# Optimization experiments

Hardware: AMD Instinct MI355X
Metric: run time of the kernel (lower is better)

Reference implementation:

```python
import jax, jax.numpy as jnp
import numpy as np

B, C, T, O = 64, 256, 4096, 256
LEVELS = 5


def setup_inputs() -> dict:
    key = jax.random.key(0)
    ks = jax.random.split(key, 10)
    s = 0.05  # weight scale, avoids tanh/sigmoid saturation
    inputs = jax.random.normal(ks[0], (B, C, T), dtype=jnp.float32)
    # original-resolution lengths; k = lens // 2**(levels-1) in [1, T]
    lens = jax.random.randint(ks[1], (B,), 16, T * 2 ** (LEVELS - 1) + 1, dtype=jnp.int32)
    return {
        "inputs": inputs,
        "lens": lens,
        "levels": LEVELS,
        "W_tanh": jax.random.normal(ks[2], (C, C), dtype=jnp.float32) * s,
        "b_tanh": jax.random.normal(ks[3], (C,), dtype=jnp.float32) * s,
        "W_sigm": jax.random.normal(ks[4], (C, C), dtype=jnp.float32) * s,
        "b_sigm": jax.random.normal(ks[5], (C,), dtype=jnp.float32) * s,
        "W_w": jax.random.normal(ks[6], (O, C), dtype=jnp.float32) * s,
        "b_w": jax.random.normal(ks[7], (O,), dtype=jnp.float32) * s,
        "W_final": jax.random.normal(ks[8], (O, C), dtype=jnp.float32) * s,
        "b_final": jax.random.normal(ks[9], (O,), dtype=jnp.float32) * s,
    }


def _conv1x1(x, W, b):
    # Conv1d with kernel_size=1: [B,C,T] x [O,C] -> [B,O,T]
    return jnp.einsum('oc,bct->bot', W, x) + b[None, :, None]


def reference(inputs, lens, levels, W_tanh, b_tanh, W_sigm, b_sigm, W_w, b_w, W_final, b_final):
    tanh = jnp.tanh(_conv1x1(inputs, W_tanh, b_tanh))
    sigm = jax.nn.sigmoid(_conv1x1(inputs, W_sigm, b_sigm))
    z = _conv1x1(tanh * sigm, W_w, b_w)  # [B,O,T]
    # per-sample valid length at this feature resolution
    k = lens // (2 ** (levels - 1))  # [B]
    t = inputs.shape[2]
    mask = jnp.arange(t)[None, None, :] < k[:, None, None]  # [B,1,T]
    z = jnp.where(mask, z, -jnp.inf)
    a = jax.nn.softmax(z, axis=2)  # length-masked softmax over time
    a2 = _conv1x1(inputs, W_final, b_final) * a  # [B,O,T]
    output = jnp.sum(a2, axis=2)  # [B,O]
    return (output, a, a2)
```

## Files before the change

### kernel.cpp

```cpp
#include <hip/hip_runtime.h>
#include <math.h>

#define Bn 64
#define Cn 256
#define Tn 4096
#define On 256
#define TT 64
#define NTILE 64
#define NROW 16384

typedef float f32x4 __attribute__((ext_vector_type(4)));
typedef __bf16 bf16x8 __attribute__((ext_vector_type(8)));
typedef __bf16 bf16x4v __attribute__((ext_vector_type(4)));
typedef unsigned short u16;
typedef u16 u16x8 __attribute__((ext_vector_type(8)));

static __device__ __forceinline__ float rcpf(float x) { return __builtin_amdgcn_rcpf(x); }
static __device__ __forceinline__ float bf2f(u16 u) { return __uint_as_float(((unsigned)u) << 16); }

#if __has_builtin(__builtin_amdgcn_exp2f)
#define EXP2(x) __builtin_amdgcn_exp2f(x)
#else
#define EXP2(x) exp2f(x)
#endif

#define BAR() do { asm volatile("s_waitcnt lgkmcnt(0)" ::: "memory"); \
                   __builtin_amdgcn_s_barrier(); } while (0)

#define SC_TANH -2.8853900817779268f
#define SC_SIGM -1.4426950408889634f
#define SC_W     1.4426950408889634f

__global__ void wprep_k(const float* __restrict__ Wt, const float* __restrict__ Ws,
                        const float* __restrict__ Ww, const float* __restrict__ Wf,
                        u16* __restrict__ dst) {
  int gid = blockIdx.x * 256 + threadIdx.x;
  int w = gid >> 16, rem = gid & 65535;
  int frag = rem >> 9, lane = (rem >> 3) & 63, i = rem & 7;
  int ot = frag >> 3, kt = frag & 7;
  int row = ot * 16 + (lane & 15);
  int col = kt * 32 + ((lane >> 4) << 3) + i;
  const float* W = (w == 0) ? Wt : (w == 1) ? Ws : (w == 2) ? Ww : Wf;
  float sc = (w == 0) ? SC_TANH : (w == 1) ? SC_SIGM : (w == 2) ? SC_W : 1.0f;
  __bf16 h = (__bf16)(W[row * 256 + col] * sc);
  dst[gid] = *(u16*)&h;
}

__global__ __launch_bounds__(512, 4) void pass1_k(
    const float* __restrict__ x, const int* __restrict__ lens, const int* __restrict__ levels,
    const u16* __restrict__ wtF, const u16* __restrict__ wsF, const u16* __restrict__ wwF,
    const u16* __restrict__ wfF,
    const float* __restrict__ btp, const float* __restrict__ bsp, const float* __restrict__ bwp,
    const float* __restrict__ bfp,
    u16* __restrict__ pW, u16* __restrict__ fW,
    float* __restrict__ Sp) {
  __shared__ u16 x_lds[16384];
  __shared__ u16 g_lds[16384];
  __shared__ float bt_sh[256], bs_sh[256], bw_sh[256], bf_sh[256];

  int tile = blockIdx.x, b = blockIdx.y;
  int t0 = tile * TT;
  int tid = threadIdx.x, wid = tid >> 6, lane = tid & 63;
  int kb = lens[b] >> (levels[0] - 1);

  if (t0 >= kb) {
    if (tid < 256) Sp[(size_t)tile * NROW + b * 256 + tid] = 0.f;
    return;
  }

  if (tid < 256) {
    bt_sh[tid] = btp[tid] * SC_TANH;
    bs_sh[tid] = bsp[tid] * SC_SIGM;
    bw_sh[tid] = bwp[tid] * SC_W;
    bf_sh[tid] = bfp[tid];
  }

  const float* xb = x + (size_t)b * Cn * Tn + t0;
  #pragma unroll
  for (int it = 0; it < 8; ++it) {
    int cb = (wid + 8 * it) * 4;
    float v0 = __builtin_nontemporal_load(&xb[(size_t)(cb + 0) * Tn + lane]);
    float v1 = __builtin_nontemporal_load(&xb[(size_t)(cb + 1) * Tn + lane]);
    float v2 = __builtin_nontemporal_load(&xb[(size_t)(cb + 2) * Tn + lane]);
    float v3 = __builtin_nontemporal_load(&xb[(size_t)(cb + 3) * Tn + lane]);
    bf16x4v pk = { (__bf16)v0, (__bf16)v1, (__bf16)v2, (__bf16)v3 };
    int frag = ((cb >> 5) * 4 + (lane >> 4));
    int lfr  = ((cb >> 3) & 3) * 16 + (lane & 15);
    *(bf16x4v*)&x_lds[(frag << 9) + (lfr << 3) + (cb & 7)] = pk;
  }
  BAR();

  f32x4 accT[2][4], accS[2][4];
  #pragma unroll
  for (int j = 0; j < 2; ++j)
    #pragma unroll
    for (int n = 0; n < 4; ++n) { accT[j][n] = (f32x4)0.f; accS[j][n] = (f32x4)0.f; }

  #pragma unroll
  for (int kt = 0; kt < 8; ++kt) {
    bf16x8 bb[4];
    #pragma unroll
    for (int n = 0; n < 4; ++n)
      bb[n] = *(const bf16x8*)&x_lds[((kt * 4 + n) << 9) + (lane << 3)];
    #pragma unroll
    for (int j = 0; j < 2; ++j) {
      int ct = wid * 2 + j;
      bf16x8 at  = *(const bf16x8*)&wtF[(ct * 8 + kt) * 512 + lane * 8];
      bf16x8 as2 = *(const bf16x8*)&wsF[(ct * 8 + kt) * 512 + lane * 8];
      #pragma unroll
      for (int n = 0; n < 4; ++n) {
        accT[j][n] = __builtin_amdgcn_mfma_f32_16x16x32_bf16(at,  bb[n], accT[j][n], 0, 0, 0);
        accS[j][n] = __builtin_amdgcn_mfma_f32_16x16x32_bf16(as2, bb[n], accS[j][n], 0, 0, 0);
      }
    }
  }

  #pragma unroll
  for (int j = 0; j < 2; ++j) {
    int ct = wid * 2 + j;
    int rowbase = ct * 16 + ((lane >> 4) << 2);
    #pragma unroll
    for (int n = 0; n < 4; ++n) {
      bf16x4v pk;
      #pragma unroll
      for (int r = 0; r < 4; ++r) {
        float e1 = EXP2(accT[j][n][r] + bt_sh[rowbase + r]);
        float e2 = EXP2(accS[j][n][r] + bs_sh[rowbase + r]);
        float g = (1.f - e1) * rcpf((1.f + e1) * (1.f + e2));
        pk[r] = (__bf16)g;
      }
      int frag = ((rowbase >> 5) * 4 + n);
      int lfr  = ((rowbase >> 3) & 3) * 16 + (lane & 15);
      *(bf16x4v*)&g_lds[(frag << 9) + (lfr << 3) + (rowbase & 7)] = pk;
    }
  }
  BAR();

  f32x4 accZ[2][4], accF[2][4];
  #pragma unroll
  for (int j = 0; j < 2; ++j)
    #pragma unroll
    for (int n = 0; n < 4; ++n) { accZ[j][n] = (f32x4)0.f; accF[j][n] = (f32x4)0.f; }

  #pragma unroll
  for (int kt = 0; kt < 8; ++kt) {
    bf16x8 gg[4], xx[4];
    #pragma unroll
    for (int n = 0; n < 4; ++n) {
      gg[n] = *(const bf16x8*)&g_lds[((kt * 4 + n) << 9) + (lane << 3)];
      xx[n] = *(const bf16x8*)&x_lds[((kt * 4 + n) << 9) + (lane << 3)];
    }
    #pragma unroll
    for (int j = 0; j < 2; ++j) {
      int ct = wid * 2 + j;
      bf16x8 aw = *(const bf16x8*)&wwF[(ct * 8 + kt) * 512 + lane * 8];
      bf16x8 af = *(const bf16x8*)&wfF[(ct * 8 + kt) * 512 + lane * 8];
      #pragma unroll
      for (int n = 0; n < 4; ++n) {
        accZ[j][n] = __builtin_amdgcn_mfma_f32_16x16x32_bf16(aw, gg[n], accZ[j][n], 0, 0, 0);
        accF[j][n] = __builtin_amdgcn_mfma_f32_16x16x32_bf16(af, xx[n], accF[j][n], 0, 0, 0);
      }
    }
  }

  #pragma unroll
  for (int j = 0; j < 2; ++j) {
    int ot = wid * 2 + j;
    int rowbase = ot * 16 + ((lane >> 4) << 2);
    int oq = rowbase >> 2;
    size_t tbase = ((size_t)(b * 64 + oq)) * Tn + t0 + (lane & 15);
    float s[4] = {0.f, 0.f, 0.f, 0.f};
    #pragma unroll
    for (int n = 0; n < 4; ++n) {
      bool v = (t0 + n * 16 + (lane & 15)) < kb;
      bf16x4v pp, ff;
      #pragma unroll
      for (int r = 0; r < 4; ++r) {
        float z = accZ[j][n][r] + bw_sh[rowbase + r];
        float p = v ? EXP2(z) : 0.f;
        s[r] += p;
        pp[r] = (__bf16)p;
        ff[r] = (__bf16)(accF[j][n][r] + bf_sh[rowbase + r]);
      }
      *(bf16x4v*)&pW[(tbase + n * 16) * 4] = pp;
      *(bf16x4v*)&fW[(tbase + n * 16) * 4] = ff;
    }
    #pragma unroll
    for (int off = 1; off < 16; off <<= 1)
      #pragma unroll
      for (int r = 0; r < 4; ++r) s[r] += __shfl_xor(s[r], off, 64);
    if ((lane & 15) == 0) {
      #pragma unroll
      for (int r = 0; r < 4; ++r)
        Sp[(size_t)tile * NROW + b * 256 + rowbase + r] = s[r];
    }
  }
}

__global__ __launch_bounds__(256) void pass2_k(
    const int* __restrict__ lens, const int* __restrict__ levels,
    const u16* __restrict__ pW, const u16* __restrict__ fW,
    const float* __restrict__ Sp,
    float* __restrict__ out0, float* __restrict__ aOut, float* __restrict__ a2Out) {
  int b = blockIdx.y, oq = blockIdx.x;
  int kb = lens[b] >> (levels[0] - 1);
  int tid = threadIdx.x, wid = tid >> 6, lane = tid & 63;
  __shared__ float dsh[16];
  __shared__ float obuf[16];

  float v = Sp[(size_t)(tid >> 2) * NROW + b * 256 + oq * 4 + (tid & 3)];
  #pragma unroll
  for (int off = 4; off < 64; off <<= 1) v += __shfl_xor(v, off, 64);
  if (lane < 4) dsh[wid * 4 + lane] = v;
  __syncthreads();
  float scr[4];
  #pragma unroll
  for (int r = 0; r < 4; ++r)
    scr[r] = 1.f / (dsh[r] + dsh[4 + r] + dsh[8 + r] + dsh[12 + r]);

  size_t pbase = ((size_t)(b * 64 + oq)) * Tn;
  size_t obase0 = ((size_t)(b * 256 + oq * 4)) * Tn;
  float osum[4] = {0.f, 0.f, 0.f, 0.f};

  #pragma unroll
  for (int c = 0; c < 4; ++c) {
    int t = c * 1024 + tid * 4;
    if (t < kb) {
      u16x8 pa = *(const u16x8*)&pW[(pbase + t) * 4];
      u16x8 pb = *(const u16x8*)&pW[(pbase + t) * 4 + 8];
      u16x8 fa = *(const u16x8*)&fW[(pbase + t) * 4];
      u16x8 fb = *(const u16x8*)&fW[(pbase + t) * 4 + 8];
      bool v1 = (t + 1) < kb, v2 = (t + 2) < kb, v3 = (t + 3) < kb;
      #pragma unroll
      for (int r = 0; r < 4; ++r) {
        float a0 = bf2f(pa[r]) * scr[r];
        float a1 = v1 ? bf2f(pa[4 + r]) * scr[r] : 0.f;
        float a2_ = v2 ? bf2f(pb[r]) * scr[r] : 0.f;
        float a3 = v3 ? bf2f(pb[4 + r]) * scr[r] : 0.f;
        f32x4 av = { a0, a1, a2_, a3 };
        f32x4 a2v = { a0 * bf2f(fa[r]), a1 * bf2f(fa[4 + r]),
                      a2_ * bf2f(fb[r]), a3 * bf2f(fb[4 + r]) };
        osum[r] += a2v[0] + a2v[1] + a2v[2] + a2v[3];
        __builtin_nontemporal_store(av,  (f32x4*)&aOut[obase0 + (size_t)r * Tn + t]);
        __builtin_nontemporal_store(a2v, (f32x4*)&a2Out[obase0 + (size_t)r * Tn + t]);
      }
    } else {
      f32x4 z4 = (f32x4)0.f;
      #pragma unroll
      for (int r = 0; r < 4; ++r) {
        __builtin_nontemporal_store(z4, (f32x4*)&aOut[obase0 + (size_t)r * Tn + t]);
        __builtin_nontemporal_store(z4, (f32x4*)&a2Out[obase0 + (size_t)r * Tn + t]);
      }
    }
  }

  #pragma unroll
  for (int r = 0; r < 4; ++r) {
    float s = osum[r];
    #pragma unroll
    for (int off = 1; off < 64; off <<= 1) s += __shfl_xor(s, off, 64);
    if (lane == 0) obuf[wid * 4 + r] = s;
  }
  __syncthreads();
  if (tid < 4)
    out0[b * 256 + oq * 4 + tid] = obuf[tid] + obuf[4 + tid] + obuf[8 + tid] + obuf[12 + tid];
}

extern "C" void kernel_launch(void* const* d_in, const int* in_sizes, int n_in,
                              void* d_out, int out_size, void* d_ws, size_t ws_size,
                              hipStream_t stream) {
  const float* x    = (const float*)d_in[0];
  const int*   lens = (const int*)d_in[1];
  const int*   lev  = (const int*)d_in[2];
  const float* Wt = (const float*)d_in[3];
  const float* bt = (const float*)d_in[4];
  const float* Ws = (const float*)d_in[5];
  const float* bs = (const float*)d_in[6];
  const float* Ww = (const float*)d_in[7];
  const float* bw = (const float*)d_in[8];
  const float* Wf = (const float*)d_in[9];
  const float* bf = (const float*)d_in[10];

  u16* wsu = (u16*)d_ws;
  u16* wtF = wsu;
  u16* wsF = wsu + 65536;
  u16* wwF = wsu + 131072;
  u16* wfF = wsu + 196608;
  u16* pW  = wsu + 262144;
  u16* fW  = pW + (size_t)NROW * Tn;
  float* Sp = (float*)(fW + (size_t)NROW * Tn);

  float* out0  = (float*)d_out;
  float* aOut  = out0 + Bn * On;
  float* a2Out = aOut + (size_t)Bn * On * Tn;

  wprep_k<<<1024, 256, 0, stream>>>(Wt, Ws, Ww, Wf, wsu);
  pass1_k<<<dim3(NTILE, Bn), 512, 0, stream>>>(x, lens, lev, wtF, wsF, wwF, wfF,
                                               bt, bs, bw, bf, pW, fW, Sp);
  pass2_k<<<dim3(64, Bn), 256, 0, stream>>>(lens, lev, pW, fW, Sp, out0, aOut, a2Out);
}
```

Baseline: 249.6 us.

## Double time tile to 128 and reuse x LDS buffer for gate output

Raises the per-block time tile from 64 to 128 columns, halving the number of tiles so each weight fragment loaded from global memory is reused across twice as many time columns. To fit the larger tile in the same LDS budget, the GEMMs are reordered: the final projection runs first from x, then tanh and sigmoid, and the gated result overwrites the x buffer in two halves separated by barriers. Pass2 now guards its partial-sum reads against the smaller tile count. The larger accumulators raise register pressure and the extra barriers serialize phases, which may lower occupancy or add stalls.

```diff
diff --git a/kernel.cpp b/kernel.cpp
--- a/kernel.cpp
+++ b/kernel.cpp
@@ -5,8 +5,8 @@
 #define Cn 256
 #define Tn 4096
 #define On 256
-#define TT 64
-#define NTILE 64
+#define TT 128
+#define NTILE 32
 #define NROW 16384
 
 typedef float f32x4 __attribute__((ext_vector_type(4)));
@@ -54,8 +54,7 @@
     const float* __restrict__ bfp,
     u16* __restrict__ pW, u16* __restrict__ fW,
     float* __restrict__ Sp) {
-  __shared__ u16 x_lds[16384];
-  __shared__ u16 g_lds[16384];
+  __shared__ u16 x_lds[32768];
   __shared__ float bt_sh[256], bs_sh[256], bw_sh[256], bf_sh[256];
 
   int tile = blockIdx.x, b = blockIdx.y;
@@ -77,113 +76,184 @@
 
   const float* xb = x + (size_t)b * Cn * Tn + t0;
   #pragma unroll
-  for (int it = 0; it < 8; ++it) {
-    int cb = (wid + 8 * it) * 4;
-    float v0 = __builtin_nontemporal_load(&xb[(size_t)(cb + 0) * Tn + lane]);
-    float v1 = __builtin_nontemporal_load(&xb[(size_t)(cb + 1) * Tn + lane]);
-    float v2 = __builtin_nontemporal_load(&xb[(size_t)(cb + 2) * Tn + lane]);
-    float v3 = __builtin_nontemporal_load(&xb[(size_t)(cb + 3) * Tn + lane]);
+  for (int it = 0; it < 16; ++it) {
+    int cb = (wid + 8 * (it & 7)) << 2;
+    int t  = ((it >> 3) << 6) + lane;
+    float v0 = __builtin_nontemporal_load(&xb[(size_t)(cb + 0) * Tn + t]);
+    float v1 = __builtin_nontemporal_load(&xb[(size_t)(cb + 1) * Tn + t]);
+    float v2 = __builtin_nontemporal_load(&xb[(size_t)(cb + 2) * Tn + t]);
+    float v3 = __builtin_nontemporal_load(&xb[(size_t)(cb + 3) * Tn + t]);
     bf16x4v pk = { (__bf16)v0, (__bf16)v1, (__bf16)v2, (__bf16)v3 };
-    int frag = ((cb >> 5) * 4 + (lane >> 4));
-    int lfr  = ((cb >> 3) & 3) * 16 + (lane & 15);
+    int frag = (cb >> 5) * 8 + (t >> 4);
+    int lfr  = ((cb >> 3) & 3) * 16 + (t & 15);
     *(bf16x4v*)&x_lds[(frag << 9) + (lfr << 3) + (cb & 7)] = pk;
   }
   BAR();
 
-  f32x4 accT[2][4], accS[2][4];
+  const int wb0 = ((wid * 2 + 0) * 8) * 512 + lane * 8;
+  const int wb1 = ((wid * 2 + 1) * 8) * 512 + lane * 8;
+  const int rb0 = (wid * 2 + 0) * 16 + ((lane >> 4) << 2);
+  const int rb1 = (wid * 2 + 1) * 16 + ((lane >> 4) << 2);
+
+  {
+    f32x4 acc[2][8];
+    #pragma unroll
+    for (int j = 0; j < 2; ++j)
+      #pragma unroll
+      for (int n = 0; n < 8; ++n) acc[j][n] = (f32x4)0.f;
+    #pragma unroll
+    for (int kt = 0; kt < 8; ++kt) {
+      bf16x8 a0 = *(const bf16x8*)&wfF[wb0 + kt * 512];
+      bf16x8 a1 = *(const bf16x8*)&wfF[wb1 + kt * 512];
+      #pragma unroll
+      for (int n = 0; n < 8; ++n) {
+        bf16x8 bbn = *(const bf16x8*)&x_lds[((kt * 8 + n) << 9) + (lane << 3)];
+        acc[0][n] = __builtin_amdgcn_mfma_f32_16x16x32_bf16(a0, bbn, acc[0][n], 0, 0, 0);
+        acc[1][n] = __builtin_amdgcn_mfma_f32_16x16x32_bf16(a1, bbn, acc[1][n], 0, 0, 0);
+      }
+    }
+    #pragma unroll
+    for (int j = 0; j < 2; ++j) {
+      int rowbase = j ? rb1 : rb0;
+      int oq = rowbase >> 2;
+      size_t tbase = ((size_t)(b * 64 + oq)) * Tn + t0 + (lane & 15);
+      #pragma unroll
+      for (int n = 0; n < 8; ++n) {
+        bf16x4v ff;
+        #pragma unroll
+        for (int r = 0; r < 4; ++r) ff[r] = (__bf16)(acc[j][n][r] + bf_sh[rowbase + r]);
+        *(bf16x4v*)&fW[(tbase + n * 16) * 4] = ff;
+      }
+    }
+  }
+
+  f32x4 accT[2][8];
   #pragma unroll
   for (int j = 0; j < 2; ++j)
     #pragma unroll
-    for (int n = 0; n < 4; ++n) { accT[j][n] = (f32x4)0.f; accS[j][n] = (f32x4)0.f; }
-
+    for (int n = 0; n < 8; ++n) accT[j][n] = (f32x4)0.f;
   #pragma unroll
   for (int kt = 0; kt < 8; ++kt) {
-    bf16x8 bb[4];
-    #pragma unroll
-    for (int n = 0; n < 4; ++n)
-      bb[n] = *(const bf16x8*)&x_lds[((kt * 4 + n) << 9) + (lane << 3)];
+    bf16x8 a0 = *(const bf16x8*)&wtF[wb0 + kt * 512];
+    bf16x8 a1 = *(const bf16x8*)&wtF[wb1 + kt * 512];
+    #pragma unroll
+    for (int n = 0; n < 8; ++n) {
+      bf16x8 bbn = *(const bf16x8*)&x_lds[((kt * 8 + n) << 9) + (lane << 3)];
+      accT[0][n] = __builtin_amdgcn_mfma_f32_16x16x32_bf16(a0, bbn, accT[0][n], 0, 0, 0);
+      accT[1][n] = __builtin_amdgcn_mfma_f32_16x16x32_bf16(a1, bbn, accT[1][n], 0, 0, 0);
+    }
+  }
+
+  {
+    f32x4 accS[2][4];
+    #pragma unroll
+    for (int j = 0; j < 2; ++j)
+      #pragma unroll
+      for (int n = 0; n < 4; ++n) accS[j][n] = (f32x4)0.f;
+    #pragma unroll
+    for (int kt = 0; kt < 8; ++kt) {
+      bf16x8 a0 = *(const bf16x8*)&wsF[wb0 + kt * 512];
+      bf16x8 a1 = *(const bf16x8*)&wsF[wb1 + kt * 512];
+      #pragma unroll
+      for (int n = 0; n < 4; ++n) {
+        bf16x8 bbn = *(const bf16x8*)&x_lds[((kt * 8 + n) << 9) + (lane << 3)];
+        accS[0][n] = __builtin_amdgcn_mfma_f32_16x16x32_bf16(a0, bbn, accS[0][n], 0, 0, 0);
+        accS[1][n] = __builtin_amdgcn_mfma_f32_16x16x32_bf16(a1, bbn, accS[1][n], 0, 0, 0);
+      }
+    }
+    BAR();
     #pragma unroll
     for (int j = 0; j < 2; ++j) {
-      int ct = wid * 2 + j;
-      bf16x8 at  = *(const bf16x8*)&wtF[(ct * 8 + kt) * 512 + lane * 8];
-      bf16x8 as2 = *(const bf16x8*)&wsF[(ct * 8 + kt) * 512 + lane * 8];
+      int rowbase = j ? rb1 : rb0;
       #pragma unroll
       for (int n = 0; n < 4; ++n) {
-        accT[j][n] = __builtin_amdgcn_mfma_f32_16x16x32_bf16(at,  bb[n], accT[j][n], 0, 0, 0);
-        accS[j][n] = __builtin_amdgcn_mfma_f32_16x16x32_bf16(as2, bb[n], accS[j][n], 0, 0, 0);
-      }
+        bf16x4v pk;
+        #pragma unroll
+        for (int r = 0; r < 4; ++r) {
+          float e1 = EXP2(accT[j][n][r] + bt_sh[rowbase + r]);
+          float e2 = EXP2(accS[j][n][r] + bs_sh[rowbase + r]);
+          pk[r] = (__bf16)((1.f - e1) * rcpf((1.f + e1) * (1.f + e2)));
+        }
+        int frag = (rowbase >> 5) * 8 + n;
+        int lfr  = ((rowbase >> 3) & 3) * 16 + (lane & 15);
+        *(bf16x4v*)&x_lds[(frag << 9) + (lfr << 3) + (rowbase & 7)] = pk;
+      }
+    }
+  }
+
+  {
+    f32x4 accS[2][4];
+    #pragma unroll
+    for (int j = 0; j < 2; ++j)
+      #pragma unroll
+      for (int n = 0; n < 4; ++n) accS[j][n] = (f32x4)0.f;
+    #pragma unroll
+    for (int kt = 0; kt < 8; ++kt) {
+      bf16x8 a0 = *(const bf16x8*)&wsF[wb0 + kt * 512];
+      bf16x8 a1 = *(const bf16x8*)&wsF[wb1 + kt * 512];
+      #pragma unroll
+      for (int n = 0; n < 4; ++n) {
+        bf16x8 bbn = *(const bf16x8*)&x_lds[((kt * 8 + n + 4) << 9) + (lane << 3)];
+        accS[0][n] = __builtin_amdgcn_mfma_f32_16x16x32_bf16(a0, bbn, accS[0][n], 0, 0, 0);
+        accS[1][n] = __builtin_amdgcn_mfma_f32_16x16x32_bf16(a1, bbn, accS[1][n], 0, 0, 0);
+      }
+    }
+    BAR();
+    #pragma unroll
+    for (int j = 0; j < 2; ++j) {
+      int rowbase = j ? rb1 : rb0;
+      #pragma unroll
+      for (int n = 0; n < 4; ++n) {
+        bf16x4v pk;
+        #pragma unroll
+        for (int r = 0; r < 4; ++r) {
+          float e1 = EXP2(accT[j][n + 4][r] + bt_sh[rowbase + r]);
+          float e2 = EXP2(accS[j][n][r] + bs_sh[rowbase + r]);
+          pk[r] = (__bf16)((1.f - e1) * rcpf((1.f + e1) * (1.f + e2)));
+        }
+        int frag = (rowbase >> 5) * 8 + (n + 4);
+        int lfr  = ((rowbase >> 3) & 3) * 16 + (lane & 15);
+        *(bf16x4v*)&x_lds[(frag << 9) + (lfr << 3) + (rowbase & 7)] = pk;
+      }
+    }
+  }
+  BAR();
+
+  f32x4 accZ[2][8];
+  #pragma unroll
+  for (int j = 0; j < 2; ++j)
+    #pragma unroll
+    for (int n = 0; n < 8; ++n) accZ[j][n] = (f32x4)0.f;
+  #pragma unroll
+  for (int kt = 0; kt < 8; ++kt) {
+    bf16x8 a0 = *(const bf16x8*)&wwF[wb0 + kt * 512];
+    bf16x8 a1 = *(const bf16x8*)&wwF[wb1 + kt * 512];
+    #pragma unroll
+    for (int n = 0; n < 8; ++n) {
+      bf16x8 bbn = *(const bf16x8*)&x_lds[((kt * 8 + n) << 9) + (lane << 3)];
+      accZ[0][n] = __builtin_amdgcn_mfma_f32_16x16x32_bf16(a0, bbn, accZ[0][n], 0, 0, 0);
+      accZ[1][n] = __builtin_amdgcn_mfma_f32_16x16x32_bf16(a1, bbn, accZ[1][n], 0, 0, 0);
     }
   }
 
   #pragma unroll
   for (int j = 0; j < 2; ++j) {
-    int ct = wid * 2 + j;
-    int rowbase = ct * 16 + ((lane >> 4) << 2);
-    #pragma unroll
-    for (int n = 0; n < 4; ++n) {
-      bf16x4v pk;
-      #pragma unroll
-      for (int r = 0; r < 4; ++r) {
-        float e1 = EXP2(accT[j][n][r] + bt_sh[rowbase + r]);
-        float e2 = EXP2(accS[j][n][r] + bs_sh[rowbase + r]);
-        float g = (1.f - e1) * rcpf((1.f + e1) * (1.f + e2));
-        pk[r] = (__bf16)g;
-      }
-      int frag = ((rowbase >> 5) * 4 + n);
-      int lfr  = ((rowbase >> 3) & 3) * 16 + (lane & 15);
-      *(bf16x4v*)&g_lds[(frag << 9) + (lfr << 3) + (rowbase & 7)] = pk;
-    }
-  }
-  BAR();
-
-  f32x4 accZ[2][4], accF[2][4];
-  #pragma unroll
-  for (int j = 0; j < 2; ++j)
-    #pragma unroll
-    for (int n = 0; n < 4; ++n) { accZ[j][n] = (f32x4)0.f; accF[j][n] = (f32x4)0.f; }
-
-  #pragma unroll
-  for (int kt = 0; kt < 8; ++kt) {
-    bf16x8 gg[4], xx[4];
-    #pragma unroll
-    for (int n = 0; n < 4; ++n) {
-      gg[n] = *(const bf16x8*)&g_lds[((kt * 4 + n) << 9) + (lane << 3)];
-      xx[n] = *(const bf16x8*)&x_lds[((kt * 4 + n) << 9) + (lane << 3)];
-    }
-    #pragma unroll
-    for (int j = 0; j < 2; ++j) {
-      int ct = wid * 2 + j;
-      bf16x8 aw = *(const bf16x8*)&wwF[(ct * 8 + kt) * 512 + lane * 8];
-      bf16x8 af = *(const bf16x8*)&wfF[(ct * 8 + kt) * 512 + lane * 8];
-      #pragma unroll
-      for (int n = 0; n < 4; ++n) {
-        accZ[j][n] = __builtin_amdgcn_mfma_f32_16x16x32_bf16(aw, gg[n], accZ[j][n], 0, 0, 0);
-        accF[j][n] = __builtin_amdgcn_mfma_f32_16x16x32_bf16(af, xx[n], accF[j][n], 0, 0, 0);
-      }
-    }
-  }
-
-  #pragma unroll
-  for (int j = 0; j < 2; ++j) {
-    int ot = wid * 2 + j;
-    int rowbase = ot * 16 + ((lane >> 4) << 2);
+    int rowbase = j ? rb1 : rb0;
     int oq = rowbase >> 2;
     size_t tbase = ((size_t)(b * 64 + oq)) * Tn + t0 + (lane & 15);
     float s[4] = {0.f, 0.f, 0.f, 0.f};
     #pragma unroll
-    for (int n = 0; n < 4; ++n) {
+    for (int n = 0; n < 8; ++n) {
       bool v = (t0 + n * 16 + (lane & 15)) < kb;
-      bf16x4v pp, ff;
+      bf16x4v pp;
       #pragma unroll
       for (int r = 0; r < 4; ++r) {
         float z = accZ[j][n][r] + bw_sh[rowbase + r];
         float p = v ? EXP2(z) : 0.f;
         s[r] += p;
         pp[r] = (__bf16)p;
-        ff[r] = (__bf16)(accF[j][n][r] + bf_sh[rowbase + r]);
       }
       *(bf16x4v*)&pW[(tbase + n * 16) * 4] = pp;
-      *(bf16x4v*)&fW[(tbase + n * 16) * 4] = ff;
     }
     #pragma unroll
     for (int off = 1; off < 16; off <<= 1)
@@ -208,7 +278,8 @@
   __shared__ float dsh[16];
   __shared__ float obuf[16];
 
-  float v = Sp[(size_t)(tid >> 2) * NROW + b * 256 + oq * 4 + (tid & 3)];
+  float v = ((tid >> 2) < NTILE)
+              ? Sp[(size_t)(tid >> 2) * NROW + b * 256 + oq * 4 + (tid & 3)] : 0.f;
   #pragma unroll
   for (int off = 4; off < 64; off <<= 1) v += __shfl_xor(v, off, 64);
   if (lane < 4) dsh[wid * 4 + lane] = v;
```

New measurement: 380.8 us. 52.6% more time.

## Process two time tiles per block with double-buffered x prefetch

Applied to the files above, without the earlier changes.

Each pass1 block now handles two consecutive 64-step time tiles. While the first tile's tanh/sigmoid GEMM results are still in registers, the block loads the second tile's x into a second LDS buffer, so global loads overlap with compute. The final-projection GEMM is moved ahead of the gate GEMM, which lets the gate output overwrite the x buffer in place. The tradeoff is half as many blocks, which lowers parallelism, and more serialized work per block.

```diff
diff --git a/kernel.cpp b/kernel.cpp
--- a/kernel.cpp
+++ b/kernel.cpp
@@ -54,19 +54,24 @@
     const float* __restrict__ bfp,
     u16* __restrict__ pW, u16* __restrict__ fW,
     float* __restrict__ Sp) {
-  __shared__ u16 x_lds[16384];
-  __shared__ u16 g_lds[16384];
+  __shared__ u16 xbufA[16384];
+  __shared__ u16 xbufB[16384];
   __shared__ float bt_sh[256], bs_sh[256], bw_sh[256], bf_sh[256];
 
-  int tile = blockIdx.x, b = blockIdx.y;
-  int t0 = tile * TT;
+  int pair = blockIdx.x, b = blockIdx.y;
+  int tile0 = pair * 2;
+  int t0 = tile0 * TT;
   int tid = threadIdx.x, wid = tid >> 6, lane = tid & 63;
   int kb = lens[b] >> (levels[0] - 1);
 
   if (t0 >= kb) {
-    if (tid < 256) Sp[(size_t)tile * NROW + b * 256 + tid] = 0.f;
+    if (tid < 256) {
+      Sp[(size_t)tile0 * NROW + b * 256 + tid] = 0.f;
+      Sp[(size_t)(tile0 + 1) * NROW + b * 256 + tid] = 0.f;
+    }
     return;
   }
+  bool valid1 = (t0 + TT) < kb;
 
   if (tid < 256) {
     bt_sh[tid] = btp[tid] * SC_TANH;
@@ -75,126 +80,168 @@
     bf_sh[tid] = bfp[tid];
   }
 
-  const float* xb = x + (size_t)b * Cn * Tn + t0;
-  #pragma unroll
-  for (int it = 0; it < 8; ++it) {
-    int cb = (wid + 8 * it) * 4;
-    float v0 = __builtin_nontemporal_load(&xb[(size_t)(cb + 0) * Tn + lane]);
-    float v1 = __builtin_nontemporal_load(&xb[(size_t)(cb + 1) * Tn + lane]);
-    float v2 = __builtin_nontemporal_load(&xb[(size_t)(cb + 2) * Tn + lane]);
-    float v3 = __builtin_nontemporal_load(&xb[(size_t)(cb + 3) * Tn + lane]);
-    bf16x4v pk = { (__bf16)v0, (__bf16)v1, (__bf16)v2, (__bf16)v3 };
-    int frag = ((cb >> 5) * 4 + (lane >> 4));
-    int lfr  = ((cb >> 3) & 3) * 16 + (lane & 15);
-    *(bf16x4v*)&x_lds[(frag << 9) + (lfr << 3) + (cb & 7)] = pk;
-  }
+#define STAGE(dstbuf, gsrc)                                                       \
+  do { const float* xbS = (gsrc);                                                 \
+    _Pragma("unroll")                                                             \
+    for (int it = 0; it < 8; ++it) {                                              \
+      int cb = (wid + 8 * it) * 4;                                                \
+      float v0 = __builtin_nontemporal_load(&xbS[(size_t)(cb + 0) * Tn + lane]);  \
+      float v1 = __builtin_nontemporal_load(&xbS[(size_t)(cb + 1) * Tn + lane]);  \
+      float v2 = __builtin_nontemporal_load(&xbS[(size_t)(cb + 2) * Tn + lane]);  \
+      float v3 = __builtin_nontemporal_load(&xbS[(size_t)(cb + 3) * Tn + lane]);  \
+      bf16x4v pk = { (__bf16)v0, (__bf16)v1, (__bf16)v2, (__bf16)v3 };            \
+      int frag = ((cb >> 5) * 4 + (lane >> 4));                                   \
+      int lfr  = ((cb >> 3) & 3) * 16 + (lane & 15);                              \
+      *(bf16x4v*)&(dstbuf)[(frag << 9) + (lfr << 3) + (cb & 7)] = pk;             \
+    } } while (0)
+
+  STAGE(xbufA, x + (size_t)b * Cn * Tn + t0);
   BAR();
 
-  f32x4 accT[2][4], accS[2][4];
-  #pragma unroll
-  for (int j = 0; j < 2; ++j)
-    #pragma unroll
-    for (int n = 0; n < 4; ++n) { accT[j][n] = (f32x4)0.f; accS[j][n] = (f32x4)0.f; }
-
-  #pragma unroll
-  for (int kt = 0; kt < 8; ++kt) {
-    bf16x8 bb[4];
-    #pragma unroll
-    for (int n = 0; n < 4; ++n)
-      bb[n] = *(const bf16x8*)&x_lds[((kt * 4 + n) << 9) + (lane << 3)];
+  #pragma unroll
+  for (int half = 0; half < 2; ++half) {
+    u16* xb_cur = half ? xbufB : xbufA;
+    int t0h = t0 + half * TT;
+    int tileh = tile0 + half;
+    bool do_pf = (half == 0) && valid1;
+
+    {
+      f32x4 accF[2][4];
+      #pragma unroll
+      for (int j = 0; j < 2; ++j)
+        #pragma unroll
+        for (int n = 0; n < 4; ++n) accF[j][n] = (f32x4)0.f;
+      #pragma unroll
+      for (int kt = 0; kt < 8; ++kt) {
+        bf16x8 bb[4];
+        #pragma unroll
+        for (int n = 0; n < 4; ++n)
+          bb[n] = *(const bf16x8*)&xb_cur[((kt * 4 + n) << 9) + (lane << 3)];
+        #pragma unroll
+        for (int j = 0; j < 2; ++j) {
+          bf16x8 af = *(const bf16x8*)&wfF[((wid * 2 + j) * 8 + kt) * 512 + lane * 8];
+          #pragma unroll
+          for (int n = 0; n < 4; ++n)
+            accF[j][n] = __builtin_amdgcn_mfma_f32_16x16x32_bf16(af, bb[n], accF[j][n], 0, 0, 0);
+        }
+      }
+      #pragma unroll
+      for (int j = 0; j < 2; ++j) {
+        int rowbase = (wid * 2 + j) * 16 + ((lane >> 4) << 2);
+        int oq = rowbase >> 2;
+        size_t tbase = ((size_t)(b * 64 + oq)) * Tn + t0h + (lane & 15);
+        #pragma unroll
+        for (int n = 0; n < 4; ++n) {
+          bf16x4v ff;
+          #pragma unroll
+          for (int r = 0; r < 4; ++r) ff[r] = (__bf16)(accF[j][n][r] + bf_sh[rowbase + r]);
+          *(bf16x4v*)&fW[(tbase + n * 16) * 4] = ff;
+        }
+      }
+    }
+
+    f32x4 accT[2][4], accS[2][4];
+    #pragma unroll
+    for (int j = 0; j < 2; ++j)
+      #pragma unroll
+      for (int n = 0; n < 4; ++n) { accT[j][n] = (f32x4)0.f; accS[j][n] = (f32x4)0.f; }
+    #pragma unroll
+    for (int kt = 0; kt < 8; ++kt) {
+      bf16x8 bb[4];
+      #pragma unroll
+      for (int n = 0; n < 4; ++n)
+        bb[n] = *(const bf16x8*)&xb_cur[((kt * 4 + n) << 9) + (lane << 3)];
+      #pragma unroll
+      for (int j = 0; j < 2; ++j) {
+        bf16x8 at  = *(const bf16x8*)&wtF[((wid * 2 + j) * 8 + kt) * 512 + lane * 8];
+        bf16x8 as2 = *(const bf16x8*)&wsF[((wid * 2 + j) * 8 + kt) * 512 + lane * 8];
+        #pragma unroll
+        for (int n = 0; n < 4; ++n) {
+          accT[j][n] = __builtin_amdgcn_mfma_f32_16x16x32_bf16(at,  bb[n], accT[j][n], 0, 0, 0);
+          accS[j][n] = __builtin_amdgcn_mfma_f32_16x16x32_bf16(as2, bb[n], accS[j][n], 0, 0, 0);
+        }
+      }
+    }
+
+    if (do_pf) STAGE(xbufB, x + (size_t)b * Cn * Tn + (t0 + TT));
+
+    BAR();
+
     #pragma unroll
     for (int j = 0; j < 2; ++j) {
-      int ct = wid * 2 + j;
-      bf16x8 at  = *(const bf16x8*)&wtF[(ct * 8 + kt) * 512 + lane * 8];
-      bf16x8 as2 = *(const bf16x8*)&wsF[(ct * 8 + kt) * 512 + lane * 8];
+      int rowbase = (wid * 2 + j) * 16 + ((lane >> 4) << 2);
       #pragma unroll
       for (int n = 0; n < 4; ++n) {
-        accT[j][n] = __builtin_amdgcn_mfma_f32_16x16x32_bf16(at,  bb[n], accT[j][n], 0, 0, 0);
-        accS[j][n] = __builtin_amdgcn_mfma_f32_16x16x32_bf16(as2, bb[n], accS[j][n], 0, 0, 0);
-      }
-    }
-  }
-
-  #pragma unroll
-  for (int j = 0; j < 2; ++j) {
-    int ct = wid * 2 + j;
-    int rowbase = ct * 16 + ((lane >> 4) << 2);
-    #pragma unroll
-    for (int n = 0; n < 4; ++n) {
-      bf16x4v pk;
-      #pragma unroll
-      for (int r = 0; r < 4; ++r) {
-        float e1 = EXP2(accT[j][n][r] + bt_sh[rowbase + r]);
-        float e2 = EXP2(accS[j][n][r] + bs_sh[rowbase + r]);
-        float g = (1.f - e1) * rcpf((1.f + e1) * (1.f + e2));
-        pk[r] = (__bf16)g;
-      }
-      int frag = ((rowbase >> 5) * 4 + n);
-      int lfr  = ((rowbase >> 3) & 3) * 16 + (lane & 15);
-      *(bf16x4v*)&g_lds[(frag << 9) + (lfr << 3) + (rowbase & 7)] = pk;
-    }
-  }
-  BAR();
-
-  f32x4 accZ[2][4], accF[2][4];
-  #pragma unroll
-  for (int j = 0; j < 2; ++j)
-    #pragma unroll
-    for (int n = 0; n < 4; ++n) { accZ[j][n] = (f32x4)0.f; accF[j][n] = (f32x4)0.f; }
-
-  #pragma unroll
-  for (int kt = 0; kt < 8; ++kt) {
-    bf16x8 gg[4], xx[4];
-    #pragma unroll
-    for (int n = 0; n < 4; ++n) {
-      gg[n] = *(const bf16x8*)&g_lds[((kt * 4 + n) << 9) + (lane << 3)];
-      xx[n] = *(const bf16x8*)&x_lds[((kt * 4 + n) << 9) + (lane << 3)];
-    }
+        bf16x4v pk;
+        #pragma unroll
+        for (int r = 0; r < 4; ++r) {
+          float e1 = EXP2(accT[j][n][r] + bt_sh[rowbase + r]);
+          float e2 = EXP2(accS[j][n][r] + bs_sh[rowbase + r]);
+          pk[r] = (__bf16)((1.f - e1) * rcpf((1.f + e1) * (1.f + e2)));
+        }
+        int frag = ((rowbase >> 5) * 4 + n);
+        int lfr  = ((rowbase >> 3) & 3) * 16 + (lane & 15);
+        *(bf16x4v*)&xb_cur[(frag << 9) + (lfr << 3) + (rowbase & 7)] = pk;
+      }
+    }
+    BAR();
+
+    f32x4 accZ[2][4];
+    #pragma unroll
+    for (int j = 0; j < 2; ++j)
+      #pragma unroll
+      for (int n = 0; n < 4; ++n) accZ[j][n] = (f32x4)0.f;
+    #pragma unroll
+    for (int kt = 0; kt < 8; ++kt) {
+      bf16x8 gg[4];
+      #pragma unroll
+      for (int n = 0; n < 4; ++n)
+        gg[n] = *(const bf16x8*)&xb_cur[((kt * 4 + n) << 9) + (lane << 3)];
+      #pragma unroll
+      for (int j = 0; j < 2; ++j) {
+        bf16x8 aw = *(const bf16x8*)&wwF[((wid * 2 + j) * 8 + kt) * 512 + lane * 8];
+        #pragma unroll
+        for (int n = 0; n < 4; ++n)
+          accZ[j][n] = __builtin_amdgcn_mfma_f32_16x16x32_bf16(aw, gg[n], accZ[j][n], 0, 0, 0);
+      }
+    }
+
     #pragma unroll
     for (int j = 0; j < 2; ++j) {
-      int ct = wid * 2 + j;
-      bf16x8 aw = *(const bf16x8*)&wwF[(ct * 8 + kt) * 512 + lane * 8];
-      bf16x8 af = *(const bf16x8*)&wfF[(ct * 8 + kt) * 512 + lane * 8];
+      int rowbase = (wid * 2 + j) * 16 + ((lane >> 4) << 2);
+      int oq = rowbase >> 2;
+      size_t tbase = ((size_t)(b * 64 + oq)) * Tn + t0h + (lane & 15);
+      float s[4] = {0.f, 0.f, 0.f, 0.f};
       #pragma unroll
       for (int n = 0; n < 4; ++n) {
-        accZ[j][n] = __builtin_amdgcn_mfma_f32_16x16x32_bf16(aw, gg[n], accZ[j][n], 0, 0, 0);
-        accF[j][n] = __builtin_amdgcn_mfma_f32_16x16x32_bf16(af, xx[n], accF[j][n], 0, 0, 0);
-      }
-    }
-  }
-
-  #pragma unroll
-  for (int j = 0; j < 2; ++j) {
-    int ot = wid * 2 + j;
-    int rowbase = ot * 16 + ((lane >> 4) << 2);
-    int oq = rowbase >> 2;
-    size_t tbase = ((size_t)(b * 64 + oq)) * Tn + t0 + (lane & 15);
-    float s[4] = {0.f, 0.f, 0.f, 0.f};
-    #pragma unroll
-    for (int n = 0; n < 4; ++n) {
-      bool v = (t0 + n * 16 + (lane & 15)) < kb;
-      bf16x4v pp, ff;
-      #pragma unroll
-      for (int r = 0; r < 4; ++r) {
-        float z = accZ[j][n][r] + bw_sh[rowbase + r];
-        float p = v ? EXP2(z) : 0.f;
-        s[r] += p;
-        pp[r] = (__bf16)p;
-        ff[r] = (__bf16)(accF[j][n][r] + bf_sh[rowbase + r]);
-      }
-      *(bf16x4v*)&pW[(tbase + n * 16) * 4] = pp;
-      *(bf16x4v*)&fW[(tbase + n * 16) * 4] = ff;
-    }
-    #pragma unroll
-    for (int off = 1; off < 16; off <<= 1)
-      #pragma unroll
-      for (int r = 0; r < 4; ++r) s[r] += __shfl_xor(s[r], off, 64);
-    if ((lane & 15) == 0) {
-      #pragma unroll
-      for (int r = 0; r < 4; ++r)
-        Sp[(size_t)tile * NROW + b * 256 + rowbase + r] = s[r];
-    }
-  }
+        bool v = (t0h + n * 16 + (lane & 15)) < kb;
+        bf16x4v pp;
+        #pragma unroll
+        for (int r = 0; r < 4; ++r) {
+          float z = accZ[j][n][r] + bw_sh[rowbase + r];
+          float p = v ? EXP2(z) : 0.f;
+          s[r] += p;
+          pp[r] = (__bf16)p;
+        }
+        *(bf16x4v*)&pW[(tbase + n * 16) * 4] = pp;
+      }
+      #pragma unroll
+      for (int off = 1; off < 16; off <<= 1)
+        #pragma unroll
+        for (int r = 0; r < 4; ++r) s[r] += __shfl_xor(s[r], off, 64);
+      if ((lane & 15) == 0) {
+        #pragma unroll
+        for (int r = 0; r < 4; ++r)
+          Sp[(size_t)tileh * NROW + b * 256 + rowbase + r] = s[r];
+      }
+    }
+
+    if (half == 0 && !valid1) {
+      if (tid < 256) Sp[(size_t)(tile0 + 1) * NROW + b * 256 + tid] = 0.f;
+      return;
+    }
+  }
+#undef STAGE
 }
 
 __global__ __launch_bounds__(256) void pass2_k(
@@ -295,7 +342,7 @@
   float* a2Out = aOut + (size_t)Bn * On * Tn;
 
   wprep_k<<<1024, 256, 0, stream>>>(Wt, Ws, Ww, Wf, wsu);
-  pass1_k<<<dim3(NTILE, Bn), 512, 0, stream>>>(x, lens, lev, wtF, wsF, wwF, wfF,
-                                               bt, bs, bw, bf, pW, fW, Sp);
+  pass1_k<<<dim3(NTILE / 2, Bn), 512, 0, stream>>>(x, lens, lev, wtF, wsF, wwF, wfF,
+                                                   bt, bs, bw, bf, pW, fW, Sp);
   pass2_k<<<dim3(64, Bn), 256, 0, stream>>>(lens, lev, pW, fW, Sp, out0, aOut, a2Out);
 }
```

Result: slower. 502.3 us (+101.2%).
